# Kernel optimization log

Measured on AMD Instinct MI355X. Metric: run time of the kernel, lower is better.

## Reference

```python
import jax, jax.numpy as jnp
import numpy as np

N_NODES = 50000
N_EDGES = 800000
IN_CH, HID_CH, OUT_CH, HEADS = 64, 32, 64, 8
NEG_SLOPE = 0.2


def setup_inputs() -> dict:
    key = jax.random.key(0)
    ks = jax.random.split(key, 12)
    x = jax.random.normal(ks[0], (N_NODES, IN_CH), dtype=jnp.float32)
    src = jax.random.randint(ks[1], (N_EDGES,), 0, N_NODES)
    dst = jax.random.randint(ks[2], (N_EDGES,), 0, N_NODES)
    edge_index = jnp.stack([src, dst]).astype(jnp.int64)
    g1 = 1.0 / np.sqrt(IN_CH)
    g2 = 1.0 / np.sqrt(HID_CH * HEADS)
    W1 = jax.random.normal(ks[3], (IN_CH, HEADS * HID_CH), dtype=jnp.float32) * g1
    a1_src = jax.random.normal(ks[4], (HEADS, HID_CH), dtype=jnp.float32) * g1
    a1_dst = jax.random.normal(ks[5], (HEADS, HID_CH), dtype=jnp.float32) * g1
    b1 = jnp.zeros((HEADS * HID_CH,), dtype=jnp.float32)
    W2 = jax.random.normal(ks[6], (HEADS * HID_CH, OUT_CH), dtype=jnp.float32) * g2
    a2_src = jax.random.normal(ks[7], (1, OUT_CH), dtype=jnp.float32) * g2
    a2_dst = jax.random.normal(ks[8], (1, OUT_CH), dtype=jnp.float32) * g2
    b2 = jnp.zeros((OUT_CH,), dtype=jnp.float32)
    return {"x": x, "edge_index": edge_index, "W1": W1, "a1_src": a1_src,
            "a1_dst": a1_dst, "b1": b1, "W2": W2, "a2_src": a2_src,
            "a2_dst": a2_dst, "b2": b2}


def _gat_conv(x, src, dst, W, a_s, a_d, b, heads, out_ch, concat):
    """PyG GATConv: per-head linear, edge attention, segment softmax, scatter-add."""
    n = x.shape[0]
    h = (x @ W).reshape(n, heads, out_ch)                    # [N,H,C]
    al_s = jnp.einsum('nhc,hc->nh', h, a_s)                  # [N,H]
    al_d = jnp.einsum('nhc,hc->nh', h, a_d)
    e = jax.nn.leaky_relu(al_s[src] + al_d[dst], NEG_SLOPE)  # [E,H]
    m = jax.ops.segment_max(e, dst, num_segments=n)          # [N,H]
    m = jnp.where(jnp.isfinite(m), m, 0.0)
    ex = jnp.exp(e - m[dst])
    denom = jax.ops.segment_sum(ex, dst, num_segments=n)
    alpha = ex / (denom[dst] + 1e-16)                        # [E,H]
    msg = h[src] * alpha[:, :, None]                         # [E,H,C]
    out = jax.ops.segment_sum(msg, dst, num_segments=n)      # [N,H,C]
    out = out.reshape(n, heads * out_ch) if concat else out.mean(axis=1)
    return out + b


def reference(x, edge_index, W1, a1_src, a1_dst, b1, W2, a2_src, a2_dst, b2):
    n = x.shape[0]
    loops = jnp.arange(n, dtype=edge_index.dtype)
    src = jnp.concatenate([edge_index[0], loops])  # self-loops (PyG default)
    dst = jnp.concatenate([edge_index[1], loops])
    h = _gat_conv(x, src, dst, W1, a1_src, a1_dst, b1, HEADS, HID_CH, True)
    h = jax.nn.elu(h)
    return _gat_conv(h, src, dst, W2, a2_src, a2_dst, b2, 1, OUT_CH, False)
```

## Files before the change

### kernel.cpp

```cpp
#include <hip/hip_runtime.h>
#include <hip/hip_fp16.h>

#define NEG_SLOPE 0.2f
#define EPB 4096
#define CAP_B 2560

typedef unsigned int uint4v __attribute__((ext_vector_type(4)));
typedef float float4v __attribute__((ext_vector_type(4)));

__global__ __launch_bounds__(256, 4) void k_phase1(
    const int* __restrict__ ei, int E,
    const float* __restrict__ x, const float* __restrict__ W1,
    const float* __restrict__ a1s, const float* __restrict__ a1d,
    __half* __restrict__ h1h, float* __restrict__ al1s, float* __restrict__ al1d,
    int* __restrict__ cursor, unsigned* __restrict__ pairs,
    int n, int nbuck, int nP1B)
{
  __shared__ int sh[2048];
  int t = threadIdx.x;
  if (blockIdx.x < nP1B) {
    int* hist = sh;
    int* hbase = sh + 512;
    for (int i = t; i < nbuck; i += 256) hist[i] = 0;
    __syncthreads();
    int ebase = blockIdx.x * EPB;
    int pk[16], bk[16], rk[16];
#pragma unroll
    for (int k = 0; k < 16; k++) {
      int eid = ebase + k * 256 + t;
      bk[k] = -1; pk[k] = 0; rk[k] = 0;
      if (eid < E) {
        int s = ei[eid], d = ei[E + eid];
        s = (s < 0) ? 0 : (s >= n ? n - 1 : s);
        d = (d < 0) ? 0 : (d >= n ? n - 1 : d);
        bk[k] = d >> 7;
        pk[k] = ((d & 127) << 17) | s;
        rk[k] = atomicAdd(&hist[d >> 7], 1);
      }
    }
    __syncthreads();
    for (int b = t; b < nbuck; b += 256) {
      int c = hist[b];
      hbase[b] = c ? atomicAdd(&cursor[b], c) : 0;
    }
    __syncthreads();
#pragma unroll
    for (int k = 0; k < 16; k++) {
      if (bk[k] >= 0) {
        int idx = hbase[bk[k]] + rk[k];
        if (idx < CAP_B)
          pairs[(size_t)bk[k] * CAP_B + idx] = (unsigned)pk[k];
      }
    }
    return;
  }
  float (*xs)[64] = reinterpret_cast<float(*)[64]>(sh);
  int cg = t & 63;
  int mg = t >> 6;
  int base = (blockIdx.x - nP1B) * 32;
  for (int i = t; i < 32 * 16; i += 256) {
    int m = i >> 4, k4 = i & 15;
    int node = base + m;
    float4 v = make_float4(0.f, 0.f, 0.f, 0.f);
    if (node < n) v = reinterpret_cast<const float4*>(x + (size_t)node * 64)[k4];
    reinterpret_cast<float4*>(&xs[m][0])[k4] = v;
  }
  float4 as4 = reinterpret_cast<const float4*>(a1s)[cg];
  float4 ad4 = reinterpret_cast<const float4*>(a1d)[cg];
  __syncthreads();
  float4 acc[8];
#pragma unroll
  for (int m = 0; m < 8; m++) acc[m] = make_float4(0.f, 0.f, 0.f, 0.f);
#pragma unroll 1
  for (int k4 = 0; k4 < 16; k4++) {
    float4 w0 = reinterpret_cast<const float4*>(W1 + (size_t)(4 * k4 + 0) * 256)[cg];
    float4 w1 = reinterpret_cast<const float4*>(W1 + (size_t)(4 * k4 + 1) * 256)[cg];
    float4 w2 = reinterpret_cast<const float4*>(W1 + (size_t)(4 * k4 + 2) * 256)[cg];
    float4 w3 = reinterpret_cast<const float4*>(W1 + (size_t)(4 * k4 + 3) * 256)[cg];
#pragma unroll
    for (int m = 0; m < 8; m++) {
      float4 xv = reinterpret_cast<float4*>(&xs[mg * 8 + m][0])[k4];
      acc[m].x = fmaf(xv.x, w0.x, acc[m].x); acc[m].y = fmaf(xv.x, w0.y, acc[m].y);
      acc[m].z = fmaf(xv.x, w0.z, acc[m].z); acc[m].w = fmaf(xv.x, w0.w, acc[m].w);
      acc[m].x = fmaf(xv.y, w1.x, acc[m].x); acc[m].y = fmaf(xv.y, w1.y, acc[m].y);
      acc[m].z = fmaf(xv.y, w1.z, acc[m].z); acc[m].w = fmaf(xv.y, w1.w, acc[m].w);
      acc[m].x = fmaf(xv.z, w2.x, acc[m].x); acc[m].y = fmaf(xv.z, w2.y, acc[m].y);
      acc[m].z = fmaf(xv.z, w2.z, acc[m].z); acc[m].w = fmaf(xv.z, w2.w, acc[m].w);
      acc[m].x = fmaf(xv.w, w3.x, acc[m].x); acc[m].y = fmaf(xv.w, w3.y, acc[m].y);
      acc[m].z = fmaf(xv.w, w3.z, acc[m].z); acc[m].w = fmaf(xv.w, w3.w, acc[m].w);
    }
  }
#pragma unroll
  for (int m = 0; m < 8; m++) {
    int node = base + mg * 8 + m;
    if (node < n) {
      int head = cg >> 3;
      __half2 p01 = __floats2half2_rn(acc[m].x, acc[m].y);
      __half2 p23 = __floats2half2_rn(acc[m].z, acc[m].w);
      uint2 pko;
      pko.x = *reinterpret_cast<unsigned int*>(&p01);
      pko.y = *reinterpret_cast<unsigned int*>(&p23);
      reinterpret_cast<uint2*>(h1h + (size_t)head * n * 32 + (size_t)node * 32)[cg & 7] = pko;
      float s_ = acc[m].x * as4.x + acc[m].y * as4.y + acc[m].z * as4.z + acc[m].w * as4.w;
      float d_ = acc[m].x * ad4.x + acc[m].y * ad4.y + acc[m].z * ad4.z + acc[m].w * ad4.w;
      s_ += __shfl_xor(s_, 1); d_ += __shfl_xor(d_, 1);
      s_ += __shfl_xor(s_, 2); d_ += __shfl_xor(d_, 2);
      s_ += __shfl_xor(s_, 4); d_ += __shfl_xor(d_, 4);
      if ((cg & 7) == 0) {
        al1s[(size_t)head * n + node] = s_;
        al1d[(size_t)head * n + node] = d_;
      }
    }
  }
}

__global__ __launch_bounds__(256) void k_pass2(
    const unsigned* __restrict__ pairs, const int* __restrict__ cursor,
    int* __restrict__ gcur, int* __restrict__ deg, int* __restrict__ rowoff,
    int* __restrict__ csr, int n)
{
  __shared__ int cnt[128], off[128], rk[128];
  __shared__ int bbase;
  int b = blockIdx.x, t = threadIdx.x;
  if (t < 128) { cnt[t] = 0; rk[t] = 0; }
  __syncthreads();
  int total = min(cursor[b], CAP_B);
  size_t base = (size_t)b * CAP_B;
  for (int i = t; i < total; i += 256)
    atomicAdd(&cnt[pairs[base + i] >> 17], 1);
  __syncthreads();
  if (t == 0) {
    int run = 0;
    for (int i = 0; i < 128; i++) { off[i] = run; run += (cnt[i] + 3) & ~3; }
    bbase = atomicAdd(gcur, run);
  }
  __syncthreads();
  int bb = bbase;
  if (t < 128) {
    int node = (b << 7) + t;
    if (node < n) {
      deg[node] = cnt[t];
      rowoff[node] = bb + off[t];
      int padded = (cnt[t] + 3) & ~3;
      for (int pp = cnt[t]; pp < padded; pp++) csr[bb + off[t] + pp] = 0;
    }
  }
  for (int i = t; i < total; i += 256) {
    unsigned p = pairs[base + i];
    int local = p >> 17;
    int slot = atomicAdd(&rk[local], 1);
    csr[bb + off[local] + slot] = (int)(p & 0x1FFFF);
  }
}

__global__ __launch_bounds__(256, 4) void k_linear2(
    const __half* __restrict__ hacth, const float* __restrict__ W2,
    const float* __restrict__ a2s, const float* __restrict__ a2d,
    __half* __restrict__ h2h, float* __restrict__ al2s, float* __restrict__ al2d,
    int n)
{
  __shared__ float xs[32][260];
  int t = threadIdx.x;
  int cg = t & 15;
  int mg = t >> 4;
  int base = blockIdx.x * 32;
  for (int i = t; i < 32 * 32; i += 256) {
    int m = i >> 5, c8 = i & 31;
    int node = base + m;
    uint4 pk = make_uint4(0, 0, 0, 0);
    if (node < n) pk = reinterpret_cast<const uint4*>(hacth + (size_t)node * 256)[c8];
    __half2* hp = reinterpret_cast<__half2*>(&pk);
    float2 f0 = __half22float2(hp[0]);
    float2 f1 = __half22float2(hp[1]);
    float2 f2 = __half22float2(hp[2]);
    float2 f3 = __half22float2(hp[3]);
    float4* dst = reinterpret_cast<float4*>(&xs[m][c8 * 8]);
    dst[0] = make_float4(f0.x, f0.y, f1.x, f1.y);
    dst[1] = make_float4(f2.x, f2.y, f3.x, f3.y);
  }
  float4 as4 = reinterpret_cast<const float4*>(a2s)[cg];
  float4 ad4 = reinterpret_cast<const float4*>(a2d)[cg];
  __syncthreads();
  float4 a0 = make_float4(0.f, 0.f, 0.f, 0.f);
  float4 a1 = make_float4(0.f, 0.f, 0.f, 0.f);
#pragma unroll 2
  for (int k4 = 0; k4 < 64; k4++) {
    float4 w0 = reinterpret_cast<const float4*>(W2 + (size_t)(4 * k4 + 0) * 64)[cg];
    float4 w1 = reinterpret_cast<const float4*>(W2 + (size_t)(4 * k4 + 1) * 64)[cg];
    float4 w2 = reinterpret_cast<const float4*>(W2 + (size_t)(4 * k4 + 2) * 64)[cg];
    float4 w3 = reinterpret_cast<const float4*>(W2 + (size_t)(4 * k4 + 3) * 64)[cg];
    float4 x0 = *reinterpret_cast<float4*>(&xs[2 * mg + 0][k4 * 4]);
    float4 x1 = *reinterpret_cast<float4*>(&xs[2 * mg + 1][k4 * 4]);
    a0.x = fmaf(x0.x, w0.x, a0.x); a0.y = fmaf(x0.x, w0.y, a0.y);
    a0.z = fmaf(x0.x, w0.z, a0.z); a0.w = fmaf(x0.x, w0.w, a0.w);
    a0.x = fmaf(x0.y, w1.x, a0.x); a0.y = fmaf(x0.y, w1.y, a0.y);
    a0.z = fmaf(x0.y, w1.z, a0.z); a0.w = fmaf(x0.y, w1.w, a0.w);
    a0.x = fmaf(x0.z, w2.x, a0.x); a0.y = fmaf(x0.z, w2.y, a0.y);
    a0.z = fmaf(x0.z, w2.z, a0.z); a0.w = fmaf(x0.z, w2.w, a0.w);
    a0.x = fmaf(x0.w, w3.x, a0.x); a0.y = fmaf(x0.w, w3.y, a0.y);
    a0.z = fmaf(x0.w, w3.z, a0.z); a0.w = fmaf(x0.w, w3.w, a0.w);
    a1.x = fmaf(x1.x, w0.x, a1.x); a1.y = fmaf(x1.x, w0.y, a1.y);
    a1.z = fmaf(x1.x, w0.z, a1.z); a1.w = fmaf(x1.x, w0.w, a1.w);
    a1.x = fmaf(x1.y, w1.x, a1.x); a1.y = fmaf(x1.y, w1.y, a1.y);
    a1.z = fmaf(x1.y, w1.z, a1.z); a1.w = fmaf(x1.y, w1.w, a1.w);
    a1.x = fmaf(x1.z, w2.x, a1.x); a1.y = fmaf(x1.z, w2.y, a1.y);
    a1.z = fmaf(x1.z, w2.z, a1.z); a1.w = fmaf(x1.z, w2.w, a1.w);
    a1.x = fmaf(x1.w, w3.x, a1.x); a1.y = fmaf(x1.w, w3.y, a1.y);
    a1.z = fmaf(x1.w, w3.z, a1.z); a1.w = fmaf(x1.w, w3.w, a1.w);
  }
#pragma unroll
  for (int nd = 0; nd < 2; nd++) {
    float4 a = nd ? a1 : a0;
    int node = base + 2 * mg + nd;
    if (node < n) {
      __half2 q0 = __floats2half2_rn(a.x, a.y);
      __half2 q1 = __floats2half2_rn(a.z, a.w);
      uint2 pk;
      pk.x = *reinterpret_cast<unsigned int*>(&q0);
      pk.y = *reinterpret_cast<unsigned int*>(&q1);
      reinterpret_cast<uint2*>(h2h + (size_t)(cg >> 3) * n * 32 + (size_t)node * 32)[cg & 7] = pk;
      float s_ = a.x * as4.x + a.y * as4.y + a.z * as4.z + a.w * as4.w;
      float d_ = a.x * ad4.x + a.y * ad4.y + a.z * ad4.z + a.w * ad4.w;
      s_ += __shfl_xor(s_, 1); d_ += __shfl_xor(d_, 1);
      s_ += __shfl_xor(s_, 2); d_ += __shfl_xor(d_, 2);
      s_ += __shfl_xor(s_, 4); d_ += __shfl_xor(d_, 4);
      s_ += __shfl_xor(s_, 8); d_ += __shfl_xor(d_, 8);
      if (cg == 0) { al2s[node] = s_; al2d[node] = d_; }
    }
  }
}

__global__ __launch_bounds__(256) void k_gather1(
    const __half* __restrict__ h1h, const float* __restrict__ al1s, const float* __restrict__ al1d,
    const int* __restrict__ degv, const int* __restrict__ rowoff, const int* __restrict__ csr,
    const float* __restrict__ b1, __half* __restrict__ hacth, int n)
{
  int head = blockIdx.x & 7;
  int node = (blockIdx.x >> 3) * 16 + (threadIdx.x >> 4);
  if (node >= n) return;
  int r = threadIdx.x & 15;
  int o = r >> 2;
  int qq = r & 3;
  const uint4* slab4 = reinterpret_cast<const uint4*>(h1h + (size_t)head * n * 32);
  const float* als = al1s + (size_t)head * n;
  float ald = al1d[(size_t)head * n + node];
  int beg = rowoff[node];
  int deg = degv[node];
  float acc[8];
#pragma unroll
  for (int k = 0; k < 8; k++) acc[k] = 0.f;
  float den = 0.f;
  int nt4 = (deg + 3) >> 2;
#pragma unroll 2
  for (int it = 0; it < nt4; it++) {
    int idx = 4 * it + o;
    int s = csr[beg + idx];
    float al = als[s];
    uint4 pv = slab4[4 * (size_t)s + qq];
    float e = al + ald;
    e = e > 0.f ? e : NEG_SLOPE * e;
    float ex = (idx < deg) ? __expf(e) : 0.f;
    den += ex;
    __half2* hp = reinterpret_cast<__half2*>(&pv);
#pragma unroll
    for (int j = 0; j < 4; j++) {
      float2 f = __half22float2(hp[j]);
      acc[2 * j + 0] = fmaf(ex, f.x, acc[2 * j + 0]);
      acc[2 * j + 1] = fmaf(ex, f.y, acc[2 * j + 1]);
    }
  }
  den += __shfl_xor(den, 4);
  den += __shfl_xor(den, 8);
#pragma unroll
  for (int k = 0; k < 8; k++) {
    acc[k] += __shfl_xor(acc[k], 4);
    acc[k] += __shfl_xor(acc[k], 8);
  }
  float eS = als[node] + ald;
  eS = eS > 0.f ? eS : NEG_SLOPE * eS;
  float exS = __expf(eS);
  den += exS;
  {
    uint4 nr = slab4[4 * (size_t)node + qq];
    __half2* hp = reinterpret_cast<__half2*>(&nr);
#pragma unroll
    for (int j = 0; j < 4; j++) {
      float2 f = __half22float2(hp[j]);
      acc[2 * j + 0] = fmaf(exS, f.x, acc[2 * j + 0]);
      acc[2 * j + 1] = fmaf(exS, f.y, acc[2 * j + 1]);
    }
  }
  if (o != 0) return;
  float inv = 1.f / (den + 1e-16f);
  const float4* bb = reinterpret_cast<const float4*>(b1 + head * 32);
  float4 b40 = bb[2 * qq], b41 = bb[2 * qq + 1];
  float ov[8];
  ov[0] = acc[0] * inv + b40.x; ov[1] = acc[1] * inv + b40.y;
  ov[2] = acc[2] * inv + b40.z; ov[3] = acc[3] * inv + b40.w;
  ov[4] = acc[4] * inv + b41.x; ov[5] = acc[5] * inv + b41.y;
  ov[6] = acc[6] * inv + b41.z; ov[7] = acc[7] * inv + b41.w;
#pragma unroll
  for (int k = 0; k < 8; k++) ov[k] = ov[k] > 0.f ? ov[k] : (__expf(ov[k]) - 1.f);
  uint4v w0;
  __half2 t0, t1;
  t0 = __floats2half2_rn(ov[0], ov[1]);  w0.x = *reinterpret_cast<unsigned int*>(&t0);
  t1 = __floats2half2_rn(ov[2], ov[3]);  w0.y = *reinterpret_cast<unsigned int*>(&t1);
  t0 = __floats2half2_rn(ov[4], ov[5]);  w0.z = *reinterpret_cast<unsigned int*>(&t0);
  t1 = __floats2half2_rn(ov[6], ov[7]);  w0.w = *reinterpret_cast<unsigned int*>(&t1);
  __builtin_nontemporal_store(
      w0, reinterpret_cast<uint4v*>(hacth + (size_t)node * 256 + head * 32 + qq * 8));
}

__global__ __launch_bounds__(256) void k_gather2(
    const __half* __restrict__ h2h, const float* __restrict__ al2s, const float* __restrict__ al2d,
    const int* __restrict__ degv, const int* __restrict__ rowoff, const int* __restrict__ csr,
    const float* __restrict__ b2, float* __restrict__ out, int n)
{
  int c = blockIdx.x & 1;
  int node = (blockIdx.x >> 1) * 16 + (threadIdx.x >> 4);
  if (node >= n) return;
  int r = threadIdx.x & 15;
  int o = r >> 2;
  int qq = r & 3;
  const uint4* slab4 = reinterpret_cast<const uint4*>(h2h + (size_t)c * n * 32);
  float ald = al2d[node];
  int beg = rowoff[node];
  int deg = degv[node];
  float acc[8];
#pragma unroll
  for (int k = 0; k < 8; k++) acc[k] = 0.f;
  float den = 0.f;
  int nt4 = (deg + 3) >> 2;
#pragma unroll 2
  for (int it = 0; it < nt4; it++) {
    int idx = 4 * it + o;
    int s = csr[beg + idx];
    float al = al2s[s];
    uint4 pv = slab4[4 * (size_t)s + qq];
    float e = al + ald;
    e = e > 0.f ? e : NEG_SLOPE * e;
    float ex = (idx < deg) ? __expf(e) : 0.f;
    den += ex;
    __half2* hp = reinterpret_cast<__half2*>(&pv);
#pragma unroll
    for (int j = 0; j < 4; j++) {
      float2 f = __half22float2(hp[j]);
      acc[2 * j + 0] = fmaf(ex, f.x, acc[2 * j + 0]);
      acc[2 * j + 1] = fmaf(ex, f.y, acc[2 * j + 1]);
    }
  }
  den += __shfl_xor(den, 4);
  den += __shfl_xor(den, 8);
#pragma unroll
  for (int k = 0; k < 8; k++) {
    acc[k] += __shfl_xor(acc[k], 4);
    acc[k] += __shfl_xor(acc[k], 8);
  }
  float eS = al2s[node] + ald;
  eS = eS > 0.f ? eS : NEG_SLOPE * eS;
  float exS = __expf(eS);
  den += exS;
  {
    uint4 nr = slab4[4 * (size_t)node + qq];
    __half2* hp = reinterpret_cast<__half2*>(&nr);
#pragma unroll
    for (int j = 0; j < 4; j++) {
      float2 f = __half22float2(hp[j]);
      acc[2 * j + 0] = fmaf(exS, f.x, acc[2 * j + 0]);
      acc[2 * j + 1] = fmaf(exS, f.y, acc[2 * j + 1]);
    }
  }
  if (o != 0) return;
  float inv = 1.f / (den + 1e-16f);
  const float4* bb = reinterpret_cast<const float4*>(b2 + c * 32);
  float4 b40 = bb[2 * qq], b41 = bb[2 * qq + 1];
  float* op = out + (size_t)node * 64 + c * 32 + qq * 8;
  float4v o0, o1;
  o0.x = acc[0] * inv + b40.x; o0.y = acc[1] * inv + b40.y;
  o0.z = acc[2] * inv + b40.z; o0.w = acc[3] * inv + b40.w;
  o1.x = acc[4] * inv + b41.x; o1.y = acc[5] * inv + b41.y;
  o1.z = acc[6] * inv + b41.z; o1.w = acc[7] * inv + b41.w;
  __builtin_nontemporal_store(o0, reinterpret_cast<float4v*>(op));
  __builtin_nontemporal_store(o1, reinterpret_cast<float4v*>(op) + 1);
}

extern "C" void kernel_launch(void* const* d_in, const int* in_sizes, int n_in,
                              void* d_out, int out_size, void* d_ws, size_t ws_size,
                              hipStream_t stream)
{
  const float* x        = (const float*)d_in[0];
  const int*   ei       = (const int*)d_in[1];
  const float* W1       = (const float*)d_in[2];
  const float* a1s      = (const float*)d_in[3];
  const float* a1d      = (const float*)d_in[4];
  const float* b1       = (const float*)d_in[5];
  const float* W2       = (const float*)d_in[6];
  const float* a2s      = (const float*)d_in[7];
  const float* a2d      = (const float*)d_in[8];
  const float* b2       = (const float*)d_in[9];
  float* out            = (float*)d_out;

  int N  = in_sizes[0] / 64;
  int E  = in_sizes[1] / 2;
  int NBUCK = (N + 127) >> 7;

  char* p = (char*)d_ws;
  auto alloc = [&](size_t bytes) -> char* {
    char* r = p;
    p += (bytes + 255) & ~(size_t)255;
    return r;
  };
  __half* h1h    = (__half*)alloc((size_t)N * 256 * 2);
  __half* hacth  = (__half*)alloc((size_t)N * 256 * 2);
  float* al1s    = (float*)alloc((size_t)N * 8 * 4);
  float* al1d    = (float*)alloc((size_t)N * 8 * 4);
  float* al2s    = (float*)alloc((size_t)N * 4);
  float* al2d    = (float*)alloc((size_t)N * 4);
  int*   deg     = (int*)alloc((size_t)N * 4);
  int*   rowoff  = (int*)alloc((size_t)N * 4);
  int*   csr     = (int*)alloc((size_t)NBUCK * CAP_B * 4);
  unsigned* pairs = (unsigned*)alloc((size_t)NBUCK * CAP_B * 4);
  int*   cursor  = (int*)alloc((size_t)(NBUCK + 1) * 4);
  int*   gcur    = cursor + NBUCK;
  __half* h2h    = h1h;

  hipMemsetAsync(cursor, 0, (size_t)(NBUCK + 1) * 4, stream);

  int nP1B = (E + EPB - 1) / EPB;
  int nLB = (N + 31) / 32;
  k_phase1<<<nP1B + nLB, 256, 0, stream>>>(ei, E, x, W1, a1s, a1d,
                                           h1h, al1s, al1d, cursor, pairs, N, NBUCK, nP1B);
  k_pass2<<<NBUCK, 256, 0, stream>>>(pairs, cursor, gcur, deg, rowoff, csr, N);
  int nG1 = 8 * ((N + 15) / 16);
  k_gather1<<<nG1, 256, 0, stream>>>(h1h, al1s, al1d, deg, rowoff, csr, b1, hacth, N);
  k_linear2<<<(N + 31) / 32, 256, 0, stream>>>(hacth, W2, a2s, a2d, h2h, al2s, al2d, N);
  int nG2 = 2 * ((N + 15) / 16);
  k_gather2<<<nG2, 256, 0, stream>>>(h2h, al2s, al2d, deg, rowoff, csr, b2, out, N);
}
```

Measured before the change: 207.0 us.

## Precompute layer-1 edge attention weights in a separate kernel before gather

Adds a kernel that computes the exponentiated leaky-relu attention weight for every CSR edge slot and head, writing them to a new per-head weight buffer. The layer-1 gather then streams these weights with nontemporal loads, which removes the dependent random lookup of al1s[s] and the exp from its inner loop, and its unroll factor is raised from 2 to 4. The cost is an extra launch, plus an 8-head weight buffer that is written once and read once, adding global memory traffic. The new kernel still performs the random al1s gathers, so the same latency is moved rather than removed.

```diff
diff --git a/kernel.cpp b/kernel.cpp
--- a/kernel.cpp
+++ b/kernel.cpp
@@ -150,6 +150,30 @@
     int local = p >> 17;
     int slot = atomicAdd(&rk[local], 1);
     csr[bb + off[local] + slot] = (int)(p & 0x1FFFF);
+  }
+}
+
+__global__ __launch_bounds__(256) void k_expw1(
+    const float* __restrict__ al1s, const float* __restrict__ al1d,
+    const int* __restrict__ degv, const int* __restrict__ rowoff, const int* __restrict__ csr,
+    float* __restrict__ w1, int slotcap, int n)
+{
+  int head = blockIdx.x & 7;
+  int node = (blockIdx.x >> 3) * 64 + (threadIdx.x >> 2);
+  if (node >= n) return;
+  int r = threadIdx.x & 3;
+  const float* als = al1s + (size_t)head * n;
+  float ald = al1d[(size_t)head * n + node];
+  int beg = rowoff[node];
+  int deg = degv[node];
+  int degpad = (deg + 3) & ~3;
+  float* wrow = w1 + (size_t)head * slotcap + beg;
+  const int* crow = csr + beg;
+  for (int idx = r; idx < degpad; idx += 4) {
+    int s = crow[idx];
+    float e = als[s] + ald;
+    e = e > 0.f ? e : NEG_SLOPE * e;
+    wrow[idx] = (idx < deg) ? __expf(e) : 0.f;
   }
 }
 
@@ -233,7 +257,8 @@
 __global__ __launch_bounds__(256) void k_gather1(
     const __half* __restrict__ h1h, const float* __restrict__ al1s, const float* __restrict__ al1d,
     const int* __restrict__ degv, const int* __restrict__ rowoff, const int* __restrict__ csr,
-    const float* __restrict__ b1, __half* __restrict__ hacth, int n)
+    const float* __restrict__ w1, const float* __restrict__ b1,
+    __half* __restrict__ hacth, int slotcap, int n)
 {
   int head = blockIdx.x & 7;
   int node = (blockIdx.x >> 3) * 16 + (threadIdx.x >> 4);
@@ -242,8 +267,7 @@
   int o = r >> 2;
   int qq = r & 3;
   const uint4* slab4 = reinterpret_cast<const uint4*>(h1h + (size_t)head * n * 32);
-  const float* als = al1s + (size_t)head * n;
-  float ald = al1d[(size_t)head * n + node];
+  const float* wrow = w1 + (size_t)head * slotcap;
   int beg = rowoff[node];
   int deg = degv[node];
   float acc[8];
@@ -251,22 +275,19 @@
   for (int k = 0; k < 8; k++) acc[k] = 0.f;
   float den = 0.f;
   int nt4 = (deg + 3) >> 2;
-#pragma unroll 2
+#pragma unroll 4
   for (int it = 0; it < nt4; it++) {
-    int idx = 4 * it + o;
-    int s = csr[beg + idx];
-    float al = als[s];
+    int idx = beg + 4 * it + o;
+    int s = csr[idx];
+    float w = __builtin_nontemporal_load(wrow + idx);
     uint4 pv = slab4[4 * (size_t)s + qq];
-    float e = al + ald;
-    e = e > 0.f ? e : NEG_SLOPE * e;
-    float ex = (idx < deg) ? __expf(e) : 0.f;
-    den += ex;
+    den += w;
     __half2* hp = reinterpret_cast<__half2*>(&pv);
 #pragma unroll
     for (int j = 0; j < 4; j++) {
       float2 f = __half22float2(hp[j]);
-      acc[2 * j + 0] = fmaf(ex, f.x, acc[2 * j + 0]);
-      acc[2 * j + 1] = fmaf(ex, f.y, acc[2 * j + 1]);
+      acc[2 * j + 0] = fmaf(w, f.x, acc[2 * j + 0]);
+      acc[2 * j + 1] = fmaf(w, f.y, acc[2 * j + 1]);
     }
   }
   den += __shfl_xor(den, 4);
@@ -276,7 +297,8 @@
     acc[k] += __shfl_xor(acc[k], 4);
     acc[k] += __shfl_xor(acc[k], 8);
   }
-  float eS = als[node] + ald;
+  const float* als = al1s + (size_t)head * n;
+  float eS = als[node] + al1d[(size_t)head * n + node];
   eS = eS > 0.f ? eS : NEG_SLOPE * eS;
   float exS = __expf(eS);
   den += exS;
@@ -403,6 +425,7 @@
   int N  = in_sizes[0] / 64;
   int E  = in_sizes[1] / 2;
   int NBUCK = (N + 127) >> 7;
+  int SLOTCAP = NBUCK * CAP_B;
 
   char* p = (char*)d_ws;
   auto alloc = [&](size_t bytes) -> char* {
@@ -418,8 +441,9 @@
   float* al2d    = (float*)alloc((size_t)N * 4);
   int*   deg     = (int*)alloc((size_t)N * 4);
   int*   rowoff  = (int*)alloc((size_t)N * 4);
-  int*   csr     = (int*)alloc((size_t)NBUCK * CAP_B * 4);
-  unsigned* pairs = (unsigned*)alloc((size_t)NBUCK * CAP_B * 4);
+  int*   csr     = (int*)alloc((size_t)SLOTCAP * 4);
+  unsigned* pairs = (unsigned*)alloc((size_t)SLOTCAP * 4);
+  float* w1      = (float*)alloc((size_t)8 * SLOTCAP * 4);
   int*   cursor  = (int*)alloc((size_t)(NBUCK + 1) * 4);
   int*   gcur    = cursor + NBUCK;
   __half* h2h    = h1h;
@@ -431,8 +455,11 @@
   k_phase1<<<nP1B + nLB, 256, 0, stream>>>(ei, E, x, W1, a1s, a1d,
                                            h1h, al1s, al1d, cursor, pairs, N, NBUCK, nP1B);
   k_pass2<<<NBUCK, 256, 0, stream>>>(pairs, cursor, gcur, deg, rowoff, csr, N);
+  int nEW = 8 * ((N + 63) / 64);
+  k_expw1<<<nEW, 256, 0, stream>>>(al1s, al1d, deg, rowoff, csr, w1, SLOTCAP, N);
   int nG1 = 8 * ((N + 15) / 16);
-  k_gather1<<<nG1, 256, 0, stream>>>(h1h, al1s, al1d, deg, rowoff, csr, b1, hacth, N);
+  k_gather1<<<nG1, 256, 0, stream>>>(h1h, al1s, al1d, deg, rowoff, csr, w1, b1,
+                                     hacth, SLOTCAP, N);
   k_linear2<<<(N + 31) / 32, 256, 0, stream>>>(hacth, W2, a2s, a2d, h2h, al2s, al2d, N);
   int nG2 = 2 * ((N + 15) / 16);
   k_gather2<<<nG2, 256, 0, stream>>>(h2h, al2s, al2d, deg, rowoff, csr, b2, out, N);
```

Result: slower. 252.7 us (+22.1%).
